# Kernel tuning notes

Measured on AMD Instinct MI355X. Metric: run time of the kernel, lower is better.

The kernel has to match this reference:

```python
import jax, jax.numpy as jnp
import numpy as np

TOP_K = 4

def _silu_and_mul(gu):
    g, u = jnp.split(gu, 2, axis=-1)
    return jax.nn.silu(g) * u

def setup_inputs() -> dict:
    key = jax.random.key(0)
    ks = jax.random.split(key, 7)
    H, E, I, Is = 2048, 16, 1408, 5632
    s = 0.02
    return {
        "hidden_states": jax.random.normal(ks[0], (4, 1024, H), dtype=jnp.float32),
        "gate_w": jax.random.normal(ks[1], (E, H), dtype=jnp.float32) * s,
        "sgate_w": jax.random.normal(ks[2], (1, H), dtype=jnp.float32) * s,
        "w13": jax.random.normal(ks[3], (E, 2 * I, H), dtype=jnp.float32) * s,
        "w2": jax.random.normal(ks[4], (E, H, I), dtype=jnp.float32) * s,
        "shared_gate_up_w": jax.random.normal(ks[5], (2 * Is, H), dtype=jnp.float32) * s,
        "shared_down_w": jax.random.normal(ks[6], (H, Is), dtype=jnp.float32) * s,
    }

def reference(hidden_states, gate_w, sgate_w, w13, w2, shared_gate_up_w, shared_down_w):
    B, S, H = hidden_states.shape
    x = hidden_states.reshape(-1, H)  # [M, H]
    E = gate_w.shape[0]

    # shared expert: SiluAndMul MLP gated by sigmoid(shared_expert_gate(x))
    shared = _silu_and_mul(x @ shared_gate_up_w.T) @ shared_down_w.T
    shared = shared * jax.nn.sigmoid(x @ sgate_w.T)  # [M, H]

    # router: softmax in fp32, top-k (NOT renormalized, per original code)
    router_logits = x @ gate_w.T
    routing_weights = jax.nn.softmax(router_logits.astype(jnp.float32), axis=-1)
    topk_w, topk_ids = jax.lax.top_k(routing_weights, TOP_K)  # [M, K]

    # loop over fixed expert set via scan; every token goes through each
    # expert, masked by its routing coefficient (0 if not routed)
    def body(acc, ew):
        w13_e, w2_e, e = ew
        coef = jnp.sum(jnp.where(topk_ids == e, topk_w, 0.0), axis=-1)  # [M]
        h = _silu_and_mul(x @ w13_e.T)  # [M, I]
        acc = acc + (h @ w2_e.T).astype(jnp.float32) * coef[:, None]
        return acc, None

    init = jnp.zeros((x.shape[0], H), dtype=jnp.float32)
    sparse_out, _ = jax.lax.scan(body, init, (w13, w2, jnp.arange(E)))
    out = shared + sparse_out.astype(x.dtype)
    return out.reshape(B, S, H)
```

## Files before the change

### kernel.cpp

```cpp
#include <hip/hip_runtime.h>
#include <hip/hip_bf16.h>

#define E_NUM 16
#define TOPK 4
#define H_DIM 2048
#define I_DIM 1408
#define IS_DIM 5632
#define M_TOK 4096

typedef __attribute__((ext_vector_type(8))) short short8;
typedef __attribute__((ext_vector_type(4))) float f32x4;

static __device__ __forceinline__ unsigned short f2bf(float f) {
    unsigned int u = __float_as_uint(f);
    unsigned int r = (u + 0x7FFFu + ((u >> 16) & 1u)) >> 16;
    return (unsigned short)r;
}

__global__ __launch_bounds__(256) void k_router(
    const float* __restrict__ x, const float* __restrict__ gw,
    const float* __restrict__ sgw, int* __restrict__ counts,
    int* __restrict__ ltok, float* __restrict__ lcoef, float* __restrict__ sg)
{
    const int wid = threadIdx.x >> 6, lane = threadIdx.x & 63;
    const int t = blockIdx.x * 4 + wid;
    const float* xr = x + (size_t)t * H_DIM;
    float xv[32];
#pragma unroll
    for (int i = 0; i < 32; ++i) xv[i] = xr[i * 64 + lane];

    float lg[E_NUM];
    for (int e = 0; e < E_NUM; ++e) {
        const float* g = gw + (size_t)e * H_DIM;
        float s = 0.f;
#pragma unroll
        for (int i = 0; i < 32; ++i) s += xv[i] * g[i * 64 + lane];
#pragma unroll
        for (int off = 32; off; off >>= 1) s += __shfl_xor(s, off);
        lg[e] = s;
    }
    {
        float s = 0.f;
#pragma unroll
        for (int i = 0; i < 32; ++i) s += xv[i] * sgw[i * 64 + lane];
#pragma unroll
        for (int off = 32; off; off >>= 1) s += __shfl_xor(s, off);
        if (lane == 0) sg[t] = 1.f / (1.f + __expf(-s));
    }
    float mx = lg[0];
#pragma unroll
    for (int e = 1; e < E_NUM; ++e) mx = fmaxf(mx, lg[e]);
    float sum = 0.f, w[E_NUM];
#pragma unroll
    for (int e = 0; e < E_NUM; ++e) { w[e] = __expf(lg[e] - mx); sum += w[e]; }
    float inv = 1.f / sum;
#pragma unroll
    for (int e = 0; e < E_NUM; ++e) w[e] *= inv;

    if (lane == 0) {
        for (int j = 0; j < TOPK; ++j) {
            float best = -1.f; int bi = 0;
            for (int e = 0; e < E_NUM; ++e) if (w[e] > best) { best = w[e]; bi = e; }
            int pos = atomicAdd(&counts[bi], 1);
            ltok[bi * M_TOK + pos]  = t;
            lcoef[bi * M_TOK + pos] = best;
            w[bi] = -2.f;
        }
    }
}

__global__ void k_prefix(const int* __restrict__ counts, int* __restrict__ base) {
    if (threadIdx.x == 0) {
        int a = 0;
        for (int e = 0; e < E_NUM; ++e) { base[e] = a; a += counts[e]; }
        base[E_NUM] = a;
    }
}

__global__ __launch_bounds__(256) void k_cvt(const float* __restrict__ x,
                                             unsigned short* __restrict__ xb)
{
    size_t i = ((size_t)blockIdx.x * 256 + threadIdx.x) * 8;
    float4 a = *(const float4*)(x + i);
    float4 b = *(const float4*)(x + i + 4);
    union { unsigned short u[8]; short8 v; } o;
    o.u[0] = f2bf(a.x); o.u[1] = f2bf(a.y); o.u[2] = f2bf(a.z); o.u[3] = f2bf(a.w);
    o.u[4] = f2bf(b.x); o.u[5] = f2bf(b.y); o.u[6] = f2bf(b.z); o.u[7] = f2bf(b.w);
    *(short8*)(xb + i) = o.v;
}

template<int MODE, int BN, int KDIM, int NOFF, int OSTR, long long BSTR>
__global__ __launch_bounds__(256) void k_gemm(
    const unsigned short* __restrict__ Abase,
    const float* __restrict__ Bbase,
    void* __restrict__ outp,
    const int* __restrict__ ltok, const float* __restrict__ lcoef,
    const int* __restrict__ counts, const int* __restrict__ basearr,
    const float* __restrict__ sg)
{
    constexpr bool DUAL = (MODE == 0 || MODE == 2);
    constexpr int NFR = BN / 32;

    const int tid = threadIdx.x;
    const int lane = tid & 63, wid = tid >> 6;
    const int wr = wid >> 1, wc = wid & 1;
    const int lr = lane & 15, lk = lane >> 4;
    const int n0 = blockIdx.x * BN;
    const int r0 = blockIdx.y * 128;
    const int e = blockIdx.z;

    int cnt = M_TOK, gbase = 0;
    if constexpr (MODE == 2 || MODE == 3) {
        cnt = counts[e];
        if (r0 >= cnt) return;
        gbase = basearr[e];
    }
    const float* Bexp = Bbase + (size_t)e * (size_t)BSTR;

    __shared__ unsigned short sA[128 * 64];
    __shared__ unsigned short sB[128 * 64];

    f32x4 acc[4][NFR];
    f32x4 accu[4][NFR];
    const f32x4 z = {0.f, 0.f, 0.f, 0.f};
#pragma unroll
    for (int m = 0; m < 4; ++m)
#pragma unroll
        for (int n = 0; n < NFR; ++n) { acc[m][n] = z; if constexpr (DUAL) accu[m][n] = z; }

#pragma unroll 1
    for (int kt = 0; kt < KDIM; kt += 64) {
#pragma unroll
        for (int i = 0; i < 4; ++i) {
            int c = i * 256 + tid;
            int row = c >> 3, c8 = c & 7;
            int ar;
            if constexpr (MODE == 0 || MODE == 1) ar = r0 + row;
            else if constexpr (MODE == 2) {
                int rr = r0 + row; if (rr > cnt - 1) rr = cnt - 1;
                ar = ltok[e * M_TOK + rr];
            } else {
                int rr = r0 + row; if (rr > cnt - 1) rr = cnt - 1;
                ar = gbase + rr;
            }
            const unsigned short* src = Abase + (size_t)ar * KDIM + kt + c8 * 8;
            short8 v = *(const short8*)src;
            *(short8*)&sA[(row << 6) + ((c8 ^ (row & 7)) << 3)] = v;
        }
#pragma unroll
        for (int i = 0; i < 4; ++i) {
            int c = i * 256 + tid;
            int row = c >> 3, c8 = c & 7;
            int br;
            if constexpr (DUAL) br = (row >> 6) ? (NOFF + n0 + (row & 63)) : (n0 + (row & 63));
            else br = n0 + row;
            const float* bs = Bexp + (size_t)br * KDIM + kt + c8 * 8;
            float4 f0 = *(const float4*)bs;
            float4 f1 = *(const float4*)(bs + 4);
            union { unsigned short u[8]; short8 v; } o;
            o.u[0] = f2bf(f0.x); o.u[1] = f2bf(f0.y); o.u[2] = f2bf(f0.z); o.u[3] = f2bf(f0.w);
            o.u[4] = f2bf(f1.x); o.u[5] = f2bf(f1.y); o.u[6] = f2bf(f1.z); o.u[7] = f2bf(f1.w);
            *(short8*)&sB[(row << 6) + ((c8 ^ (row & 7)) << 3)] = o.v;
        }
        __syncthreads();
#pragma unroll
        for (int kk = 0; kk < 2; ++kk) {
            const int c8 = kk * 4 + lk;
            short8 af[4];
#pragma unroll
            for (int m = 0; m < 4; ++m) {
                int row = wr * 64 + m * 16 + lr;
                af[m] = *(const short8*)&sA[(row << 6) + ((c8 ^ (row & 7)) << 3)];
            }
#pragma unroll
            for (int n = 0; n < NFR; ++n) {
                int rowb = wc * (BN / 2) + n * 16 + lr;
                short8 bf = *(const short8*)&sB[(rowb << 6) + ((c8 ^ (rowb & 7)) << 3)];
#pragma unroll
                for (int m = 0; m < 4; ++m)
                    acc[m][n] = __builtin_amdgcn_mfma_f32_16x16x32_bf16(af[m], bf, acc[m][n], 0, 0, 0);
                if constexpr (DUAL) {
                    int rowu = rowb + 64;
                    short8 bu = *(const short8*)&sB[(rowu << 6) + ((c8 ^ (rowu & 7)) << 3)];
#pragma unroll
                    for (int m = 0; m < 4; ++m)
                        accu[m][n] = __builtin_amdgcn_mfma_f32_16x16x32_bf16(af[m], bu, accu[m][n], 0, 0, 0);
                }
            }
        }
        __syncthreads();
    }

    const int colbase = n0 + wc * (BN / 2);
#pragma unroll
    for (int m = 0; m < 4; ++m) {
#pragma unroll
        for (int j = 0; j < 4; ++j) {
            const int r = wr * 64 + m * 16 + lk * 4 + j;
            if constexpr (MODE == 0) {
                size_t orow = (size_t)(r0 + r) * IS_DIM;
#pragma unroll
                for (int n = 0; n < NFR; ++n) {
                    int col = colbase + n * 16 + lr;
                    float g = acc[m][n][j];
                    float h = g / (1.f + __expf(-g)) * accu[m][n][j];
                    ((unsigned short*)outp)[orow + col] = f2bf(h);
                }
            } else if constexpr (MODE == 2) {
                if (r0 + r < cnt) {
                    size_t orow = (size_t)(gbase + r0 + r) * I_DIM;
#pragma unroll
                    for (int n = 0; n < NFR; ++n) {
                        int col = colbase + n * 16 + lr;
                        float g = acc[m][n][j];
                        float h = g / (1.f + __expf(-g)) * accu[m][n][j];
                        ((unsigned short*)outp)[orow + col] = f2bf(h);
                    }
                }
            } else if constexpr (MODE == 1) {
                int tok = r0 + r;
                float scale = sg[tok];
                size_t orow = (size_t)tok * H_DIM;
#pragma unroll
                for (int n = 0; n < NFR; ++n) {
                    int col = colbase + n * 16 + lr;
                    ((float*)outp)[orow + col] = acc[m][n][j] * scale;
                }
            } else {
                if (r0 + r < cnt) {
                    int tok = ltok[e * M_TOK + r0 + r];
                    float scale = lcoef[e * M_TOK + r0 + r];
                    size_t orow = (size_t)tok * H_DIM;
#pragma unroll
                    for (int n = 0; n < NFR; ++n) {
                        int col = colbase + n * 16 + lr;
                        atomicAdd((float*)outp + orow + col, acc[m][n][j] * scale);
                    }
                }
            }
        }
    }
}

extern "C" void kernel_launch(void* const* d_in, const int* in_sizes, int n_in,
                              void* d_out, int out_size, void* d_ws, size_t ws_size,
                              hipStream_t stream) {
    const float* x    = (const float*)d_in[0];
    const float* gw   = (const float*)d_in[1];
    const float* sgw  = (const float*)d_in[2];
    const float* w13  = (const float*)d_in[3];
    const float* w2   = (const float*)d_in[4];
    const float* sguw = (const float*)d_in[5];
    const float* sdw  = (const float*)d_in[6];
    float* out = (float*)d_out;

    char* ws = (char*)d_ws;
    unsigned short* xb   = (unsigned short*)(ws);
    unsigned short* hbuf = (unsigned short*)(ws + 16777216);
    int*   ltok   = (int*)  (ws + 62914560);
    float* lcoef  = (float*)(ws + 63176704);
    int*   counts = (int*)  (ws + 63438848);
    int*   basep  = (int*)  (ws + 63439104);
    float* sg     = (float*)(ws + 63439360);

    hipMemsetAsync(counts, 0, 64, stream);
    k_router<<<M_TOK / 4, 256, 0, stream>>>(x, gw, sgw, counts, ltok, lcoef, sg);
    k_prefix<<<1, 64, 0, stream>>>(counts, basep);
    k_cvt<<<(M_TOK * H_DIM) / (256 * 8), 256, 0, stream>>>(x, xb);

    k_gemm<0, 64, 2048, 5632, 5632, 0>
        <<<dim3(IS_DIM / 64, M_TOK / 128, 1), 256, 0, stream>>>(
            xb, sguw, hbuf, ltok, lcoef, counts, basep, sg);
    k_gemm<1, 128, 5632, 0, 2048, 0>
        <<<dim3(H_DIM / 128, M_TOK / 128, 1), 256, 0, stream>>>(
            hbuf, sdw, out, ltok, lcoef, counts, basep, sg);
    k_gemm<2, 64, 2048, 1408, 1408, 5767168LL>
        <<<dim3(I_DIM / 64, M_TOK / 128, E_NUM), 256, 0, stream>>>(
            xb, w13, hbuf, ltok, lcoef, counts, basep, sg);
    k_gemm<3, 128, 1408, 0, 2048, 2883584LL>
        <<<dim3(H_DIM / 128, M_TOK / 128, E_NUM), 256, 0, stream>>>(
            hbuf, w2, out, ltok, lcoef, counts, basep, sg);
}
```

Before: 1.393 ms.

## Pre-convert weights to bf16 and load GEMM tiles via global_load_lds

Adds a separate grid-stride pass that converts all weight matrices to bf16 in workspace when it is large enough. The GEMM kernels then stage both A and B tiles with direct global-to-LDS loads and precomputed swizzled pointers, instead of converting fp32 weights in registers on every tile load. This removes redundant per-block fp32 reads and conversion work. In exchange, every call pays a full conversion pass over the weights and needs a much larger workspace, with the old path kept as a fallback.

```diff
diff --git a/kernel.cpp b/kernel.cpp
--- a/kernel.cpp
+++ b/kernel.cpp
@@ -15,6 +15,12 @@
     unsigned int u = __float_as_uint(f);
     unsigned int r = (u + 0x7FFFu + ((u >> 16) & 1u)) >> 16;
     return (unsigned short)r;
+}
+
+static __device__ __forceinline__ void gl16(const unsigned short* g, unsigned short* l) {
+    __builtin_amdgcn_global_load_lds(
+        (const __attribute__((address_space(1))) unsigned int*)g,
+        (__attribute__((address_space(3))) unsigned int*)l, 16, 0, 0);
 }
 
 __global__ __launch_bounds__(256) void k_router(
@@ -77,22 +83,25 @@
     }
 }
 
-__global__ __launch_bounds__(256) void k_cvt(const float* __restrict__ x,
-                                             unsigned short* __restrict__ xb)
+__global__ __launch_bounds__(256) void k_cvtw(const float* __restrict__ src,
+                                              unsigned short* __restrict__ dst, size_t n8)
 {
-    size_t i = ((size_t)blockIdx.x * 256 + threadIdx.x) * 8;
-    float4 a = *(const float4*)(x + i);
-    float4 b = *(const float4*)(x + i + 4);
-    union { unsigned short u[8]; short8 v; } o;
-    o.u[0] = f2bf(a.x); o.u[1] = f2bf(a.y); o.u[2] = f2bf(a.z); o.u[3] = f2bf(a.w);
-    o.u[4] = f2bf(b.x); o.u[5] = f2bf(b.y); o.u[6] = f2bf(b.z); o.u[7] = f2bf(b.w);
-    *(short8*)(xb + i) = o.v;
-}
-
-template<int MODE, int BN, int KDIM, int NOFF, int OSTR, long long BSTR>
+    size_t stride = (size_t)gridDim.x * 256;
+    for (size_t t = (size_t)blockIdx.x * 256 + threadIdx.x; t < n8; t += stride) {
+        size_t i = t * 8;
+        float4 a = *(const float4*)(src + i);
+        float4 b = *(const float4*)(src + i + 4);
+        union { unsigned short u[8]; short8 v; } o;
+        o.u[0] = f2bf(a.x); o.u[1] = f2bf(a.y); o.u[2] = f2bf(a.z); o.u[3] = f2bf(a.w);
+        o.u[4] = f2bf(b.x); o.u[5] = f2bf(b.y); o.u[6] = f2bf(b.z); o.u[7] = f2bf(b.w);
+        *(short8*)(dst + i) = o.v;
+    }
+}
+
+template<int MODE, int BN, int KDIM, int NOFF, long long BSTR, bool BCVT>
 __global__ __launch_bounds__(256) void k_gemm(
     const unsigned short* __restrict__ Abase,
-    const float* __restrict__ Bbase,
+    const void* __restrict__ Bvoid,
     void* __restrict__ outp,
     const int* __restrict__ ltok, const float* __restrict__ lcoef,
     const int* __restrict__ counts, const int* __restrict__ basearr,
@@ -115,10 +124,41 @@
         if (r0 >= cnt) return;
         gbase = basearr[e];
     }
-    const float* Bexp = Bbase + (size_t)e * (size_t)BSTR;
 
     __shared__ unsigned short sA[128 * 64];
     __shared__ unsigned short sB[128 * 64];
+
+    const int srow = lane >> 3, sc8 = lane & 7;
+    const unsigned short* aptr[4];
+#pragma unroll
+    for (int i = 0; i < 4; ++i) {
+        const int row = (i * 4 + wid) * 8 + srow;
+        int ar;
+        if constexpr (MODE == 0 || MODE == 1) ar = r0 + row;
+        else if constexpr (MODE == 2) {
+            int rr = r0 + row; if (rr > cnt - 1) rr = cnt - 1;
+            ar = ltok[e * M_TOK + rr];
+        } else {
+            int rr = r0 + row; if (rr > cnt - 1) rr = cnt - 1;
+            ar = gbase + rr;
+        }
+        aptr[i] = Abase + (size_t)ar * KDIM + ((sc8 ^ (row & 7)) << 3);
+    }
+    const unsigned short* bptr[4];
+    const float* Bf = nullptr;
+    if constexpr (BCVT) {
+        const unsigned short* Bx = (const unsigned short*)Bvoid + (size_t)e * (size_t)BSTR;
+#pragma unroll
+        for (int i = 0; i < 4; ++i) {
+            const int row = (i * 4 + wid) * 8 + srow;
+            int br;
+            if constexpr (DUAL) br = (row >= 64) ? (NOFF + n0 + row - 64) : (n0 + row);
+            else br = n0 + row;
+            bptr[i] = Bx + (size_t)br * KDIM + ((sc8 ^ (row & 7)) << 3);
+        }
+    } else {
+        Bf = (const float*)Bvoid + (size_t)e * (size_t)BSTR;
+    }
 
     f32x4 acc[4][NFR];
     f32x4 accu[4][NFR];
@@ -131,36 +171,28 @@
 #pragma unroll 1
     for (int kt = 0; kt < KDIM; kt += 64) {
 #pragma unroll
-        for (int i = 0; i < 4; ++i) {
-            int c = i * 256 + tid;
-            int row = c >> 3, c8 = c & 7;
-            int ar;
-            if constexpr (MODE == 0 || MODE == 1) ar = r0 + row;
-            else if constexpr (MODE == 2) {
-                int rr = r0 + row; if (rr > cnt - 1) rr = cnt - 1;
-                ar = ltok[e * M_TOK + rr];
-            } else {
-                int rr = r0 + row; if (rr > cnt - 1) rr = cnt - 1;
-                ar = gbase + rr;
+        for (int i = 0; i < 4; ++i)
+            gl16(aptr[i] + kt, &sA[(i * 4 + wid) * 512]);
+        if constexpr (BCVT) {
+#pragma unroll
+            for (int i = 0; i < 4; ++i)
+                gl16(bptr[i] + kt, &sB[(i * 4 + wid) * 512]);
+        } else {
+#pragma unroll
+            for (int i = 0; i < 4; ++i) {
+                int c = i * 256 + tid;
+                int row = c >> 3, c8 = c & 7;
+                int br;
+                if constexpr (DUAL) br = (row >= 64) ? (NOFF + n0 + row - 64) : (n0 + row);
+                else br = n0 + row;
+                const float* bs = Bf + (size_t)br * KDIM + kt + c8 * 8;
+                float4 f0 = *(const float4*)bs;
+                float4 f1 = *(const float4*)(bs + 4);
+                union { unsigned short u[8]; short8 v; } o;
+                o.u[0] = f2bf(f0.x); o.u[1] = f2bf(f0.y); o.u[2] = f2bf(f0.z); o.u[3] = f2bf(f0.w);
+                o.u[4] = f2bf(f1.x); o.u[5] = f2bf(f1.y); o.u[6] = f2bf(f1.z); o.u[7] = f2bf(f1.w);
+                *(short8*)&sB[(row << 6) + ((c8 ^ (row & 7)) << 3)] = o.v;
             }
-            const unsigned short* src = Abase + (size_t)ar * KDIM + kt + c8 * 8;
-            short8 v = *(const short8*)src;
-            *(short8*)&sA[(row << 6) + ((c8 ^ (row & 7)) << 3)] = v;
-        }
-#pragma unroll
-        for (int i = 0; i < 4; ++i) {
-            int c = i * 256 + tid;
-            int row = c >> 3, c8 = c & 7;
-            int br;
-            if constexpr (DUAL) br = (row >> 6) ? (NOFF + n0 + (row & 63)) : (n0 + (row & 63));
-            else br = n0 + row;
-            const float* bs = Bexp + (size_t)br * KDIM + kt + c8 * 8;
-            float4 f0 = *(const float4*)bs;
-            float4 f1 = *(const float4*)(bs + 4);
-            union { unsigned short u[8]; short8 v; } o;
-            o.u[0] = f2bf(f0.x); o.u[1] = f2bf(f0.y); o.u[2] = f2bf(f0.z); o.u[3] = f2bf(f0.w);
-            o.u[4] = f2bf(f1.x); o.u[5] = f2bf(f1.y); o.u[6] = f2bf(f1.z); o.u[7] = f2bf(f1.w);
-            *(short8*)&sB[(row << 6) + ((c8 ^ (row & 7)) << 3)] = o.v;
         }
         __syncthreads();
 #pragma unroll
@@ -255,29 +287,55 @@
     float* out = (float*)d_out;
 
     char* ws = (char*)d_ws;
-    unsigned short* xb   = (unsigned short*)(ws);
+    unsigned short* xb   = (unsigned short*)ws;
     unsigned short* hbuf = (unsigned short*)(ws + 16777216);
-    int*   ltok   = (int*)  (ws + 62914560);
-    float* lcoef  = (float*)(ws + 63176704);
-    int*   counts = (int*)  (ws + 63438848);
-    int*   basep  = (int*)  (ws + 63439104);
-    float* sg     = (float*)(ws + 63439360);
+    const bool full = (ws_size >= 409485824ULL);
+    unsigned short* w13b  = (unsigned short*)(ws + 62914560);
+    unsigned short* w2b   = (unsigned short*)(ws + 247463936);
+    unsigned short* sguwb = (unsigned short*)(ws + 339738624);
+    unsigned short* sdwb  = (unsigned short*)(ws + 385875968);
+    size_t so = full ? 408944640ULL : 62914560ULL;
+    int*   ltok   = (int*)  (ws + so);
+    float* lcoef  = (float*)(ws + so + 262144);
+    int*   counts = (int*)  (ws + so + 524288);
+    int*   basep  = (int*)  (ws + so + 524288 + 256);
+    float* sg     = (float*)(ws + so + 524288 + 512);
 
     hipMemsetAsync(counts, 0, 64, stream);
     k_router<<<M_TOK / 4, 256, 0, stream>>>(x, gw, sgw, counts, ltok, lcoef, sg);
     k_prefix<<<1, 64, 0, stream>>>(counts, basep);
-    k_cvt<<<(M_TOK * H_DIM) / (256 * 8), 256, 0, stream>>>(x, xb);
-
-    k_gemm<0, 64, 2048, 5632, 5632, 0>
-        <<<dim3(IS_DIM / 64, M_TOK / 128, 1), 256, 0, stream>>>(
-            xb, sguw, hbuf, ltok, lcoef, counts, basep, sg);
-    k_gemm<1, 128, 5632, 0, 2048, 0>
-        <<<dim3(H_DIM / 128, M_TOK / 128, 1), 256, 0, stream>>>(
-            hbuf, sdw, out, ltok, lcoef, counts, basep, sg);
-    k_gemm<2, 64, 2048, 1408, 1408, 5767168LL>
-        <<<dim3(I_DIM / 64, M_TOK / 128, E_NUM), 256, 0, stream>>>(
-            xb, w13, hbuf, ltok, lcoef, counts, basep, sg);
-    k_gemm<3, 128, 1408, 0, 2048, 2883584LL>
-        <<<dim3(H_DIM / 128, M_TOK / 128, E_NUM), 256, 0, stream>>>(
-            hbuf, w2, out, ltok, lcoef, counts, basep, sg);
-}
+    k_cvtw<<<4096, 256, 0, stream>>>(x, xb, (size_t)M_TOK * H_DIM / 8);
+
+    if (full) {
+        k_cvtw<<<8192, 256, 0, stream>>>(sguw, sguwb, (size_t)2 * IS_DIM * H_DIM / 8);
+        k_cvtw<<<8192, 256, 0, stream>>>(sdw,  sdwb,  (size_t)H_DIM * IS_DIM / 8);
+        k_cvtw<<<8192, 256, 0, stream>>>(w13,  w13b,  (size_t)E_NUM * 2 * I_DIM * H_DIM / 8);
+        k_cvtw<<<8192, 256, 0, stream>>>(w2,   w2b,   (size_t)E_NUM * H_DIM * I_DIM / 8);
+
+        k_gemm<0, 64, 2048, IS_DIM, 0, true>
+            <<<dim3(IS_DIM / 64, M_TOK / 128, 1), 256, 0, stream>>>(
+                xb, sguwb, hbuf, ltok, lcoef, counts, basep, sg);
+        k_gemm<1, 128, 5632, 0, 0, true>
+            <<<dim3(H_DIM / 128, M_TOK / 128, 1), 256, 0, stream>>>(
+                hbuf, sdwb, out, ltok, lcoef, counts, basep, sg);
+        k_gemm<2, 64, 2048, I_DIM, 5767168LL, true>
+            <<<dim3(I_DIM / 64, M_TOK / 128, E_NUM), 256, 0, stream>>>(
+                xb, w13b, hbuf, ltok, lcoef, counts, basep, sg);
+        k_gemm<3, 128, 1408, 0, 2883584LL, true>
+            <<<dim3(H_DIM / 128, M_TOK / 128, E_NUM), 256, 0, stream>>>(
+                hbuf, w2b, out, ltok, lcoef, counts, basep, sg);
+    } else {
+        k_gemm<0, 64, 2048, IS_DIM, 0, false>
+            <<<dim3(IS_DIM / 64, M_TOK / 128, 1), 256, 0, stream>>>(
+                xb, sguw, hbuf, ltok, lcoef, counts, basep, sg);
+        k_gemm<1, 128, 5632, 0, 0, false>
+            <<<dim3(H_DIM / 128, M_TOK / 128, 1), 256, 0, stream>>>(
+                hbuf, sdw, out, ltok, lcoef, counts, basep, sg);
+        k_gemm<2, 64, 2048, I_DIM, 5767168LL, false>
+            <<<dim3(I_DIM / 64, M_TOK / 128, E_NUM), 256, 0, stream>>>(
+                xb, w13, hbuf, ltok, lcoef, counts, basep, sg);
+        k_gemm<3, 128, 1408, 0, 2883584LL, false>
+            <<<dim3(H_DIM / 128, M_TOK / 128, E_NUM), 256, 0, stream>>>(
+                hbuf, w2, out, ltok, lcoef, counts, basep, sg);
+    }
+}
```

Result: faster. 1.337 ms (-4.1%).
